# Kernel optimization log

Hardware: AMD Instinct MI355X
Metric: run time of the kernel (lower is better)

## Reference

```python
import math
import jax, jax.numpy as jnp
import numpy as np

B, L, D, H, DFF = 2, 2048, 1024, 16, 4096
HD = D // H
NUM_BUCKETS, MAX_DISTANCE = 32, 128


def setup_inputs() -> dict:
    key = jax.random.key(0)
    ks = jax.random.split(key, 10)
    s = 0.02
    return {
        "hidden_states": jax.random.normal(ks[0], (B, L, D), dtype=jnp.float32),
        "Wq": jax.random.normal(ks[1], (D, D), dtype=jnp.float32) * s,
        "Wk": jax.random.normal(ks[2], (D, D), dtype=jnp.float32) * s,
        "Wv": jax.random.normal(ks[3], (D, D), dtype=jnp.float32) * s,
        "Wo": jax.random.normal(ks[4], (D, D), dtype=jnp.float32) * s,
        "W1": jax.random.normal(ks[5], (D, DFF), dtype=jnp.float32) * s,
        "W2": jax.random.normal(ks[6], (DFF, D), dtype=jnp.float32) * s,
        "ln1_g": jnp.ones((D,), dtype=jnp.float32),
        "ln2_g": jnp.ones((D,), dtype=jnp.float32),
        "rel_table": jax.random.normal(ks[7], (NUM_BUCKETS, H), dtype=jnp.float32) * s,
    }


def rms_norm(x, g, eps=1e-6):
    # T5-style LayerNorm: scale only, no mean subtraction
    var = jnp.mean(jnp.square(x.astype(jnp.float32)), axis=-1, keepdims=True)
    return (x.astype(jnp.float32) * jax.lax.rsqrt(var + eps)).astype(x.dtype) * g


def relative_position_bias(seq_len, table):
    # bidirectional T5 bucket scheme, num_buckets=32, max_distance=128
    ctx = jnp.arange(seq_len)[:, None]
    mem = jnp.arange(seq_len)[None, :]
    rp = mem - ctx                                  # (L, L) int
    nb = NUM_BUCKETS // 2
    buckets = (rp > 0).astype(jnp.int32) * nb
    rpa = jnp.abs(rp)
    max_exact = nb // 2
    is_small = rpa < max_exact
    safe = jnp.maximum(rpa, 1).astype(jnp.float32)  # avoid log(0); masked by is_small
    large = max_exact + (
        jnp.log(safe / max_exact) / math.log(MAX_DISTANCE / max_exact) * (nb - max_exact)
    ).astype(jnp.int32)
    large = jnp.minimum(large, nb - 1)
    buckets = buckets + jnp.where(is_small, rpa, large)   # (L, L)
    vals = table[buckets]                                  # (L, L, H)
    return jnp.transpose(vals, (2, 0, 1))[None]            # (1, H, L, L)


def reference(hidden_states, Wq, Wk, Wv, Wo, W1, W2, ln1_g, ln2_g, rel_table):
    x = hidden_states
    b, l, d = x.shape

    # --- self-attention sublayer (pre-norm) ---
    h = rms_norm(x, ln1_g)
    q = (h @ Wq).reshape(b, l, H, HD)
    k = (h @ Wk).reshape(b, l, H, HD)
    v = (h @ Wv).reshape(b, l, H, HD)

    bias = relative_position_bias(l, rel_table)            # (1, H, L, L)
    # NOTE: source's manual attention path has NO 1/sqrt(head_dim) scaling
    scores = jnp.einsum("bqhd,bkhd->bhqk", q, k) + bias
    attn = jax.nn.softmax(scores.astype(jnp.float32), axis=-1).astype(scores.dtype)
    out = jnp.einsum("bhqk,bkhd->bqhd", attn, v).reshape(b, l, d)
    x = x + out @ Wo

    # --- feed-forward sublayer (pre-norm) ---
    h = rms_norm(x, ln2_g)
    x = x + jax.nn.relu(h @ W1) @ W2
    return x
```

## Files before the change

kernel.cpp:

```cpp
#include <hip/hip_runtime.h>
#include <hip/hip_bf16.h>
#include <math.h>

#define BDIM 1024
#define HEADS 16
#define HDIM 64
#define LSEQ 2048
#define NBATCH 2
#define DFFDIM 4096
#define QKVN 3072

typedef __bf16 bf16x8_t __attribute__((ext_vector_type(8)));
typedef float f32x4_t __attribute__((ext_vector_type(4)));

__device__ __forceinline__ ushort f2bf(float f) {
    union { __hip_bfloat16 b; ushort u; } cv;
    cv.b = __float2bfloat16(f);
    return cv.u;
}
__device__ __forceinline__ float bf2f(ushort u) {
    union { unsigned int i; float f; } cv;
    cv.i = ((unsigned int)u) << 16;
    return cv.f;
}

__global__ __launch_bounds__(256) void transpose_cvt(const float* __restrict__ W,
                                                     ushort* __restrict__ Wt,
                                                     int K, int N) {
    __shared__ ushort tile[32][33];
    int bi = blockIdx.y;
    int bj = blockIdx.x;
    int tx = threadIdx.x;
    int ty = threadIdx.y;
#pragma unroll
    for (int r = 0; r < 4; ++r) {
        int krow = bi * 32 + ty + r * 8;
        int ncol = bj * 32 + tx;
        tile[ty + r * 8][tx] = f2bf(W[(size_t)krow * N + ncol]);
    }
    __syncthreads();
#pragma unroll
    for (int r = 0; r < 4; ++r) {
        int nrow = bj * 32 + ty + r * 8;
        int kcol = bi * 32 + tx;
        Wt[(size_t)nrow * K + kcol] = tile[tx][ty + r * 8];
    }
}

__global__ __launch_bounds__(256) void vtrans(const ushort* __restrict__ qkv,
                                              ushort* __restrict__ vT) {
    __shared__ ushort t[64][72];
    const int ktile = blockIdx.x;
    const int bh = blockIdx.y;
    const int b = bh >> 4, h = bh & 15;
    const int tid = threadIdx.x;
    const int r = tid >> 2;
    const int c0 = (tid & 3) * 16;
    const ushort* src = qkv + (size_t)(b * LSEQ + ktile * 64 + r) * QKVN + 2048 + h * HDIM + c0;
    union { bf16x8_t v; ushort s[8]; } u0, u1;
    u0.v = *(const bf16x8_t*)src;
    u1.v = *(const bf16x8_t*)(src + 8);
#pragma unroll
    for (int j = 0; j < 8; ++j) { t[r][c0 + j] = u0.s[j]; t[r][c0 + 8 + j] = u1.s[j]; }
    __syncthreads();
    const int hd = tid >> 2;
    union { bf16x8_t v; ushort s[8]; } w0, w1;
#pragma unroll
    for (int j = 0; j < 8; ++j) { w0.s[j] = t[c0 + j][hd]; w1.s[j] = t[c0 + 8 + j][hd]; }
    ushort* dst = vT + (size_t)(bh * HDIM + hd) * LSEQ + ktile * 64 + c0;
    *(bf16x8_t*)dst = w0.v;
    *(bf16x8_t*)(dst + 8) = w1.v;
}

__global__ __launch_bounds__(256) void rmsnorm_k(const float* __restrict__ x,
                                                 const float* __restrict__ g,
                                                 ushort* __restrict__ out) {
    int row = blockIdx.x;
    int t = threadIdx.x;
    int w = t >> 6, l = t & 63;
    const float4 v = reinterpret_cast<const float4*>(x + (size_t)row * BDIM)[t];
    float ss = v.x * v.x + v.y * v.y + v.z * v.z + v.w * v.w;
#pragma unroll
    for (int m = 1; m <= 32; m <<= 1) ss += __shfl_xor(ss, m);
    __shared__ float wsum[4];
    if (l == 0) wsum[w] = ss;
    __syncthreads();
    float tot = wsum[0] + wsum[1] + wsum[2] + wsum[3];
    float r = rsqrtf(tot * (1.0f / BDIM) + 1e-6f);
    const float4 gv = reinterpret_cast<const float4*>(g)[t];
    ushort4 o;
    o.x = f2bf(v.x * r * gv.x);
    o.y = f2bf(v.y * r * gv.y);
    o.z = f2bf(v.z * r * gv.z);
    o.w = f2bf(v.w * r * gv.w);
    reinterpret_cast<ushort4*>(out + (size_t)row * BDIM)[t] = o;
}

__global__ void bias_table_k(const float* __restrict__ rel, float* __restrict__ btab) {
    int idx = blockIdx.x * 256 + threadIdx.x;
    if (idx >= HEADS * 4095) return;
    int h = idx / 4095;
    int d = idx % 4095;
    int rp = d - 2047;
    int bucket = rp > 0 ? 16 : 0;
    int rpa = rp < 0 ? -rp : rp;
    if (rpa < 8) {
        bucket += rpa;
    } else {
        int large = 8 + (int)(logf((float)rpa * 0.125f) * (1.0f / logf(16.0f)) * 8.0f);
        bucket += large < 15 ? large : 15;
    }
    btab[idx] = rel[bucket * HEADS + h];
}

__global__ __launch_bounds__(256) void reduce2_k(const ushort* __restrict__ parts,
                                                 const float* __restrict__ res,
                                                 float* __restrict__ out,
                                                 size_t mn) {
    size_t i = ((size_t)blockIdx.x * 256 + threadIdx.x) * 4;
    float4 r = *(const float4*)(res + i);
    ushort4 a = *(const ushort4*)(parts + i);
    ushort4 b = *(const ushort4*)(parts + mn + i);
    float4 o;
    o.x = r.x + bf2f(a.x) + bf2f(b.x);
    o.y = r.y + bf2f(a.y) + bf2f(b.y);
    o.z = r.z + bf2f(a.z) + bf2f(b.z);
    o.w = r.w + bf2f(a.w) + bf2f(b.w);
    *(float4*)(out + i) = o;
}

__global__ __launch_bounds__(256) void reduce2_rms(const ushort* __restrict__ parts,
                                                   const float* __restrict__ res,
                                                   const float* __restrict__ g,
                                                   float* __restrict__ out,
                                                   ushort* __restrict__ hout,
                                                   size_t mn) {
    int row = blockIdx.x;
    int t = threadIdx.x;
    int w = t >> 6, l = t & 63;
    size_t i = (size_t)row * BDIM + t * 4;
    float4 r = *(const float4*)(res + i);
    ushort4 a = *(const ushort4*)(parts + i);
    ushort4 b = *(const ushort4*)(parts + mn + i);
    float4 o;
    o.x = r.x + bf2f(a.x) + bf2f(b.x);
    o.y = r.y + bf2f(a.y) + bf2f(b.y);
    o.z = r.z + bf2f(a.z) + bf2f(b.z);
    o.w = r.w + bf2f(a.w) + bf2f(b.w);
    *(float4*)(out + i) = o;
    float ss = o.x * o.x + o.y * o.y + o.z * o.z + o.w * o.w;
#pragma unroll
    for (int m = 1; m <= 32; m <<= 1) ss += __shfl_xor(ss, m);
    __shared__ float wsum[4];
    if (l == 0) wsum[w] = ss;
    __syncthreads();
    float tot = wsum[0] + wsum[1] + wsum[2] + wsum[3];
    float rr = rsqrtf(tot * (1.0f / BDIM) + 1e-6f);
    const float4 gv = reinterpret_cast<const float4*>(g)[t];
    ushort4 h;
    h.x = f2bf(o.x * rr * gv.x);
    h.y = f2bf(o.y * rr * gv.y);
    h.z = f2bf(o.z * rr * gv.z);
    h.w = f2bf(o.w * rr * gv.w);
    reinterpret_cast<ushort4*>(hout + (size_t)row * BDIM)[t] = h;
}

template <int MODE, int TM, int TN>
__global__ __launch_bounds__(256) void gemm_bt(const ushort* __restrict__ A,
                                               const ushort* __restrict__ Bt,
                                               void* Cout, const float* res,
                                               int M, int N, int K, int nbx, int nkc) {
    __shared__ __align__(16) ushort As[TM * 64];
    __shared__ __align__(16) ushort Bs[TN * 64];
    constexpr int MF = TM / 32, NF = TN / 32;
    const int nwg = gridDim.x;
    const int bid = blockIdx.x;
    const int swz = (bid & 7) * (nwg >> 3) + (bid >> 3);
    const int nxy = nwg / nkc;
    const int chunk = swz / nxy;
    const int bxy = swz % nxy;
    const int bx = bxy % nbx, by = bxy / nbx;
    const int Kc = K / nkc;
    const int kbeg = chunk * Kc;
    const int tid = threadIdx.x;
    const int w = tid >> 6, l = tid & 63;
    const int wm = w >> 1, wn = w & 1;
    const int rowA0 = by * TM;
    const int colB0 = bx * TN;
    const int lr = l >> 3;
    const int scs = ((l & 7) ^ lr) * 8;
    const int c = l & 15, gq = l >> 4;
    const int rswz = (c & 7) * 8;
    f32x4_t acc[MF][NF] = {};

    auto stage = [&](int k0) {
#pragma unroll
        for (int i = 0; i < TM / 32; ++i) {
            int r = i * 32 + w * 8;
            __builtin_amdgcn_global_load_lds(
                (const __attribute__((address_space(1))) uint32_t*)(A + (size_t)(rowA0 + r + lr) * K + kbeg + k0 + scs),
                (__attribute__((address_space(3))) uint32_t*)(&As[r * 64]), 16, 0, 0);
        }
#pragma unroll
        for (int i = 0; i < TN / 32; ++i) {
            int r = i * 32 + w * 8;
            __builtin_amdgcn_global_load_lds(
                (const __attribute__((address_space(1))) uint32_t*)(Bt + (size_t)(colB0 + r + lr) * K + kbeg + k0 + scs),
                (__attribute__((address_space(3))) uint32_t*)(&Bs[r * 64]), 16, 0, 0);
        }
    };

    const int nk = Kc >> 6;
    for (int kt = 0; kt < nk; ++kt) {
        __syncthreads();
        stage(kt << 6);
        __syncthreads();
#pragma unroll
        for (int kk = 0; kk < 2; ++kk) {
            bf16x8_t av[MF], bv[NF];
#pragma unroll
            for (int mf = 0; mf < MF; ++mf)
                av[mf] = *(const bf16x8_t*)&As[(wm * (TM / 2) + mf * 16 + c) * 64 + ((kk * 32 + gq * 8) ^ rswz)];
#pragma unroll
            for (int nf = 0; nf < NF; ++nf)
                bv[nf] = *(const bf16x8_t*)&Bs[(wn * (TN / 2) + nf * 16 + c) * 64 + ((kk * 32 + gq * 8) ^ rswz)];
#pragma unroll
            for (int mf = 0; mf < MF; ++mf)
#pragma unroll
                for (int nf = 0; nf < NF; ++nf)
                    acc[mf][nf] = __builtin_amdgcn_mfma_f32_16x16x32_bf16(av[mf], bv[nf], acc[mf][nf], 0, 0, 0);
        }
    }
#pragma unroll
    for (int mf = 0; mf < MF; ++mf) {
#pragma unroll
        for (int nf = 0; nf < NF; ++nf) {
#pragma unroll
            for (int i = 0; i < 4; ++i) {
                int row = rowA0 + wm * (TM / 2) + mf * 16 + gq * 4 + i;
                int col = colB0 + wn * (TN / 2) + nf * 16 + c;
                size_t idx = (size_t)row * N + col;
                float vv = acc[mf][nf][i];
                if (MODE == 0) {
                    ((ushort*)Cout)[idx] = f2bf(vv);
                } else if (MODE == 1) {
                    ((float*)Cout)[idx] = res[idx] + vv;
                } else if (MODE == 2) {
                    ((ushort*)Cout)[idx] = f2bf(vv > 0.f ? vv : 0.f);
                } else {
                    ((ushort*)Cout)[(size_t)chunk * M * N + idx] = f2bf(vv);
                }
            }
        }
    }
}

__global__ __launch_bounds__(512) void attn_fwd(const ushort* __restrict__ qkv,
                                                const ushort* __restrict__ vT,
                                                const float* __restrict__ btab,
                                                ushort* __restrict__ ob) {
    const int tid = threadIdx.x, w = tid >> 6, l = tid & 63;
    const int bh = blockIdx.y, b = bh >> 4, h = bh & 15;
    const int qt = blockIdx.x;
    __shared__ __align__(16) ushort Ks[2][64 * 64];
    __shared__ __align__(16) ushort Vs[2][64 * 64];
    __shared__ __align__(16) ushort Pl[8][16 * 72];
    const int q0 = qt * 128 + w * 16;
    const int c = l & 15, g = l >> 4;
    const size_t rowbase = (size_t)b * LSEQ * QKVN;
    const ushort* qp = qkv + rowbase + h * HDIM;
    const ushort* kp = qkv + rowbase + BDIM + h * HDIM;
    const ushort* vtp = vT + (size_t)bh * HDIM * LSEQ;
    const int sr = tid >> 3;
    const int scs = ((l & 7) ^ (l >> 3)) * 8;
    const float* btq4 = btab + h * 4095 + 2047 - (q0 + c) + g * 4;

    bf16x8_t aq[2];
#pragma unroll
    for (int kk = 0; kk < 2; ++kk)
        aq[kk] = *(const bf16x8_t*)(qp + (size_t)(q0 + c) * QKVN + kk * 32 + g * 8);

    float lrow = 0.f;
    f32x4_t o[4] = {};
    f32x4_t s[4];

    auto stage = [&](int buf, int key0) {
        __builtin_amdgcn_global_load_lds(
            (const __attribute__((address_space(1))) uint32_t*)(kp + (size_t)(key0 + sr) * QKVN + scs),
            (__attribute__((address_space(3))) uint32_t*)(&Ks[buf][(w * 8) * 64]), 16, 0, 0);
        __builtin_amdgcn_global_load_lds(
            (const __attribute__((address_space(1))) uint32_t*)(vtp + (size_t)sr * LSEQ + key0 + scs),
            (__attribute__((address_space(3))) uint32_t*)(&Vs[buf][(w * 8) * 64]), 16, 0, 0);
    };
    auto loadBias = [&](int key0) {
#pragma unroll
        for (int nf = 0; nf < 4; ++nf)
#pragma unroll
            for (int i = 0; i < 4; ++i)
                s[nf][i] = btq4[key0 + nf * 16 + i];
    };

    stage(0, 0);
    loadBias(0);
    int cur = 0;

    ushort* Pw = Pl[w];
    const int rswz = (c & 7) << 3;
    for (int kt = 0; kt < 32; ++kt) {
        __syncthreads();
        if (kt < 31) stage(cur ^ 1, kt * 64 + 64);
#pragma unroll
        for (int kk = 0; kk < 2; ++kk)
#pragma unroll
            for (int nf = 0; nf < 4; ++nf) {
                bf16x8_t kf = *(const bf16x8_t*)&Ks[cur][(nf * 16 + c) * 64 + ((kk * 32 + g * 8) ^ rswz)];
                s[nf] = __builtin_amdgcn_mfma_f32_16x16x32_bf16(kf, aq[kk], s[nf], 0, 0, 0);
            }
        float rs = 0.f;
        union { ushort us[4]; uint2 u2; } pk[4];
#pragma unroll
        for (int nf = 0; nf < 4; ++nf)
#pragma unroll
            for (int i = 0; i < 4; ++i) {
                float pv = __expf(s[nf][i]);
                rs += pv;
                pk[nf].us[i] = f2bf(pv);
            }
        if (kt < 31) loadBias(kt * 64 + 64);
        lrow += rs;
#pragma unroll
        for (int nf = 0; nf < 4; ++nf)
            *(uint2*)&Pw[c * 72 + nf * 16 + g * 4] = pk[nf].u2;
        bf16x8_t pa[2];
#pragma unroll
        for (int kk = 0; kk < 2; ++kk)
            pa[kk] = *(const bf16x8_t*)&Pw[c * 72 + kk * 32 + g * 8];
#pragma unroll
        for (int kk = 0; kk < 2; ++kk)
#pragma unroll
            for (int hf = 0; hf < 4; ++hf) {
                bf16x8_t vf = *(const bf16x8_t*)&Vs[cur][(hf * 16 + c) * 64 + ((kk * 32 + g * 8) ^ rswz)];
                o[hf] = __builtin_amdgcn_mfma_f32_16x16x32_bf16(vf, pa[kk], o[hf], 0, 0, 0);
            }
        cur ^= 1;
    }
    lrow += __shfl_xor(lrow, 16);
    lrow += __shfl_xor(lrow, 32);
    const float inv = 1.f / lrow;
    ushort* orow = ob + (size_t)(b * LSEQ + q0 + c) * BDIM + h * HDIM + g * 4;
#pragma unroll
    for (int hf = 0; hf < 4; ++hf) {
        ushort4 ov;
        ov.x = f2bf(o[hf][0] * inv);
        ov.y = f2bf(o[hf][1] * inv);
        ov.z = f2bf(o[hf][2] * inv);
        ov.w = f2bf(o[hf][3] * inv);
        *(ushort4*)(orow + hf * 16) = ov;
    }
}

extern "C" void kernel_launch(void* const* d_in, const int* in_sizes, int n_in,
                              void* d_out, int out_size, void* d_ws, size_t ws_size,
                              hipStream_t stream) {
    const float* x   = (const float*)d_in[0];
    const float* Wq  = (const float*)d_in[1];
    const float* Wk  = (const float*)d_in[2];
    const float* Wv  = (const float*)d_in[3];
    const float* Wo  = (const float*)d_in[4];
    const float* W1  = (const float*)d_in[5];
    const float* W2  = (const float*)d_in[6];
    const float* g1  = (const float*)d_in[7];
    const float* g2  = (const float*)d_in[8];
    const float* rel = (const float*)d_in[9];
    float* out = (float*)d_out;

    char* ws = (char*)d_ws;
    const size_t MB = 1024 * 1024;
    ushort* wqkvT = (ushort*)(ws + 0 * MB);
    ushort* woT   = (ushort*)(ws + 6 * MB);
    ushort* w1T   = (ushort*)(ws + 8 * MB);
    ushort* w2T   = (ushort*)(ws + 16 * MB);
    float*  btab  = (float*)(ws + 24 * MB);
    ushort* hbuf  = (ushort*)(ws + 25 * MB);
    ushort* qkvb  = (ushort*)(ws + 33 * MB);
    ushort* woP   = (ushort*)(ws + 33 * MB);
    ushort* f1b   = (ushort*)(ws + 33 * MB);
    ushort* vTb   = (ushort*)(ws + 57 * MB);
    ushort* w2P   = (ushort*)(ws + 0 * MB);
    (void)in_sizes; (void)n_in; (void)out_size; (void)ws_size;

    const size_t MN = (size_t)4096 * 1024;
    dim3 tb(32, 8);
    transpose_cvt<<<dim3(32, 32),  tb, 0, stream>>>(Wq, wqkvT,                1024, 1024);
    transpose_cvt<<<dim3(32, 32),  tb, 0, stream>>>(Wk, wqkvT + 1024 * 1024,  1024, 1024);
    transpose_cvt<<<dim3(32, 32),  tb, 0, stream>>>(Wv, wqkvT + 2048 * 1024,  1024, 1024);
    transpose_cvt<<<dim3(32, 32),  tb, 0, stream>>>(Wo, woT, 1024, 1024);
    transpose_cvt<<<dim3(128, 32), tb, 0, stream>>>(W1, w1T, 1024, 4096);
    transpose_cvt<<<dim3(32, 128), tb, 0, stream>>>(W2, w2T, 4096, 1024);
    bias_table_k<<<256, 256, 0, stream>>>(rel, btab);

    rmsnorm_k<<<4096, 256, 0, stream>>>(x, g1, hbuf);
    gemm_bt<0, 128, 128><<<768, 256, 0, stream>>>(hbuf, wqkvT, qkvb, nullptr, 4096, QKVN, 1024, 24, 1);
    vtrans<<<dim3(32, 32), 256, 0, stream>>>(qkvb, vTb);
    attn_fwd<<<dim3(16, 32), 512, 0, stream>>>(qkvb, vTb, btab, hbuf);
    gemm_bt<3, 128, 128><<<512, 256, 0, stream>>>(hbuf, woT, woP, nullptr, 4096, 1024, 1024, 8, 2);
    reduce2_rms<<<4096, 256, 0, stream>>>(woP, x, g2, out, hbuf, MN);
    gemm_bt<2, 128, 128><<<1024, 256, 0, stream>>>(hbuf, w1T, f1b, nullptr, 4096, DFFDIM, 1024, 32, 1);
    gemm_bt<3, 128, 128><<<512, 256, 0, stream>>>(f1b, w2T, w2P, nullptr, 4096, 1024, 4096, 8, 2);
    reduce2_k<<<4096, 256, 0, stream>>>(w2P, out, out, MN);
}
```

Before: 244.3 us.

## Split attention over two key halves with a combine kernel; batch square weight transposes

Attention now runs as a split-K (flash-decoding style) kernel: each block handles half of the keys and writes unnormalised partial outputs in bf16 plus row sums, and a new combine kernel adds the two halves and normalises. This doubles the attention grid from 512 to 1024 blocks to fill more compute units. The cost is an extra kernel launch, extra global traffic for the partial outputs, and an extra bf16 rounding step. Separately, the four 1024x1024 weight transpose launches are merged into one 3D-grid launch to cut launch overhead.

New measurement: 248.6 us. Within noise of the previous version (+1.8%).

```diff
diff --git a/kernel.cpp b/kernel.cpp
--- a/kernel.cpp
+++ b/kernel.cpp
@@ -45,6 +45,29 @@
         int kcol = bi * 32 + tx;
         Wt[(size_t)nrow * K + kcol] = tile[tx][ty + r * 8];
     }
+}
+
+__global__ __launch_bounds__(256) void transpose_cvt4(const float* __restrict__ W0,
+                                                      const float* __restrict__ W1,
+                                                      const float* __restrict__ W2,
+                                                      const float* __restrict__ W3,
+                                                      ushort* __restrict__ T0,
+                                                      ushort* __restrict__ T1,
+                                                      ushort* __restrict__ T2,
+                                                      ushort* __restrict__ T3) {
+    __shared__ ushort tile[32][33];
+    const int z = blockIdx.z;
+    const float* W = z == 0 ? W0 : z == 1 ? W1 : z == 2 ? W2 : W3;
+    ushort* T = z == 0 ? T0 : z == 1 ? T1 : z == 2 ? T2 : T3;
+    int bi = blockIdx.y, bj = blockIdx.x;
+    int tx = threadIdx.x, ty = threadIdx.y;
+#pragma unroll
+    for (int r = 0; r < 4; ++r)
+        tile[ty + r * 8][tx] = f2bf(W[(size_t)(bi * 32 + ty + r * 8) * 1024 + bj * 32 + tx]);
+    __syncthreads();
+#pragma unroll
+    for (int r = 0; r < 4; ++r)
+        T[(size_t)(bj * 32 + ty + r * 8) * 1024 + bi * 32 + tx] = tile[tx][ty + r * 8];
 }
 
 __global__ __launch_bounds__(256) void vtrans(const ushort* __restrict__ qkv,
@@ -255,13 +278,16 @@
     }
 }
 
-__global__ __launch_bounds__(512) void attn_fwd(const ushort* __restrict__ qkv,
-                                                const ushort* __restrict__ vT,
-                                                const float* __restrict__ btab,
-                                                ushort* __restrict__ ob) {
+__global__ __launch_bounds__(512) void attn_fwd_split(const ushort* __restrict__ qkv,
+                                                      const ushort* __restrict__ vT,
+                                                      const float* __restrict__ btab,
+                                                      ushort* __restrict__ opart,
+                                                      float* __restrict__ lpart) {
     const int tid = threadIdx.x, w = tid >> 6, l = tid & 63;
     const int bh = blockIdx.y, b = bh >> 4, h = bh & 15;
     const int qt = blockIdx.x;
+    const int half = blockIdx.z;
+    const int keybase = half * 1024;
     __shared__ __align__(16) ushort Ks[2][64 * 64];
     __shared__ __align__(16) ushort Vs[2][64 * 64];
     __shared__ __align__(16) ushort Pl[8][16 * 72];
@@ -300,15 +326,16 @@
                 s[nf][i] = btq4[key0 + nf * 16 + i];
     };
 
-    stage(0, 0);
-    loadBias(0);
+    stage(0, keybase);
+    loadBias(keybase);
     int cur = 0;
 
     ushort* Pw = Pl[w];
     const int rswz = (c & 7) << 3;
-    for (int kt = 0; kt < 32; ++kt) {
+    for (int kt = 0; kt < 16; ++kt) {
+        const int key0 = keybase + kt * 64;
         __syncthreads();
-        if (kt < 31) stage(cur ^ 1, kt * 64 + 64);
+        if (kt < 15) stage(cur ^ 1, key0 + 64);
 #pragma unroll
         for (int kk = 0; kk < 2; ++kk)
 #pragma unroll
@@ -326,7 +353,7 @@
                 rs += pv;
                 pk[nf].us[i] = f2bf(pv);
             }
-        if (kt < 31) loadBias(kt * 64 + 64);
+        if (kt < 15) loadBias(key0 + 64);
         lrow += rs;
 #pragma unroll
         for (int nf = 0; nf < 4; ++nf)
@@ -346,17 +373,38 @@
     }
     lrow += __shfl_xor(lrow, 16);
     lrow += __shfl_xor(lrow, 32);
-    const float inv = 1.f / lrow;
-    ushort* orow = ob + (size_t)(b * LSEQ + q0 + c) * BDIM + h * HDIM + g * 4;
+    ushort* orow = opart + (size_t)half * 4194304 + (size_t)(b * LSEQ + q0 + c) * BDIM + h * HDIM + g * 4;
 #pragma unroll
     for (int hf = 0; hf < 4; ++hf) {
         ushort4 ov;
-        ov.x = f2bf(o[hf][0] * inv);
-        ov.y = f2bf(o[hf][1] * inv);
-        ov.z = f2bf(o[hf][2] * inv);
-        ov.w = f2bf(o[hf][3] * inv);
+        ov.x = f2bf(o[hf][0]);
+        ov.y = f2bf(o[hf][1]);
+        ov.z = f2bf(o[hf][2]);
+        ov.w = f2bf(o[hf][3]);
         *(ushort4*)(orow + hf * 16) = ov;
     }
+    if (l < 16) lpart[half * 65536 + bh * 2048 + q0 + c] = lrow;
+}
+
+__global__ __launch_bounds__(256) void attn_combine(const ushort* __restrict__ opart,
+                                                    const float* __restrict__ lpart,
+                                                    ushort* __restrict__ ob) {
+    const int row = blockIdx.x;
+    const int t = threadIdx.x;
+    const int b = row >> 11, q = row & 2047;
+    const int h = t >> 4;
+    const float denom = lpart[(b * 16 + h) * 2048 + q] +
+                        lpart[65536 + (b * 16 + h) * 2048 + q];
+    const float inv = 1.f / denom;
+    size_t i = (size_t)row * BDIM + t * 4;
+    ushort4 a = *(const ushort4*)(opart + i);
+    ushort4 c = *(const ushort4*)(opart + 4194304 + i);
+    ushort4 o;
+    o.x = f2bf((bf2f(a.x) + bf2f(c.x)) * inv);
+    o.y = f2bf((bf2f(a.y) + bf2f(c.y)) * inv);
+    o.z = f2bf((bf2f(a.z) + bf2f(c.z)) * inv);
+    o.w = f2bf((bf2f(a.w) + bf2f(c.w)) * inv);
+    *(ushort4*)(ob + i) = o;
 }
 
 extern "C" void kernel_launch(void* const* d_in, const int* in_sizes, int n_in,
@@ -386,15 +434,15 @@
     ushort* woP   = (ushort*)(ws + 33 * MB);
     ushort* f1b   = (ushort*)(ws + 33 * MB);
     ushort* vTb   = (ushort*)(ws + 57 * MB);
+    ushort* oPrt  = (ushort*)(ws + 65 * MB);
+    float*  lPrt  = (float*)(ws + 81 * MB);
     ushort* w2P   = (ushort*)(ws + 0 * MB);
     (void)in_sizes; (void)n_in; (void)out_size; (void)ws_size;
 
     const size_t MN = (size_t)4096 * 1024;
     dim3 tb(32, 8);
-    transpose_cvt<<<dim3(32, 32),  tb, 0, stream>>>(Wq, wqkvT,                1024, 1024);
-    transpose_cvt<<<dim3(32, 32),  tb, 0, stream>>>(Wk, wqkvT + 1024 * 1024,  1024, 1024);
-    transpose_cvt<<<dim3(32, 32),  tb, 0, stream>>>(Wv, wqkvT + 2048 * 1024,  1024, 1024);
-    transpose_cvt<<<dim3(32, 32),  tb, 0, stream>>>(Wo, woT, 1024, 1024);
+    transpose_cvt4<<<dim3(32, 32, 4), tb, 0, stream>>>(Wq, Wk, Wv, Wo,
+        wqkvT, wqkvT + 1024 * 1024, wqkvT + 2048 * 1024, woT);
     transpose_cvt<<<dim3(128, 32), tb, 0, stream>>>(W1, w1T, 1024, 4096);
     transpose_cvt<<<dim3(32, 128), tb, 0, stream>>>(W2, w2T, 4096, 1024);
     bias_table_k<<<256, 256, 0, stream>>>(rel, btab);
@@ -402,7 +450,8 @@
     rmsnorm_k<<<4096, 256, 0, stream>>>(x, g1, hbuf);
     gemm_bt<0, 128, 128><<<768, 256, 0, stream>>>(hbuf, wqkvT, qkvb, nullptr, 4096, QKVN, 1024, 24, 1);
     vtrans<<<dim3(32, 32), 256, 0, stream>>>(qkvb, vTb);
-    attn_fwd<<<dim3(16, 32), 512, 0, stream>>>(qkvb, vTb, btab, hbuf);
+    attn_fwd_split<<<dim3(16, 32, 2), 512, 0, stream>>>(qkvb, vTb, btab, oPrt, lPrt);
+    attn_combine<<<4096, 256, 0, stream>>>(oPrt, lPrt, hbuf);
     gemm_bt<3, 128, 128><<<512, 256, 0, stream>>>(hbuf, woT, woP, nullptr, 4096, 1024, 1024, 8, 2);
     reduce2_rms<<<4096, 256, 0, stream>>>(woP, x, g2, out, hbuf, MN);
     gemm_bt<2, 128, 128><<<1024, 256, 0, stream>>>(hbuf, w1T, f1b, nullptr, 4096, DFFDIM, 1024, 32, 1);
```

## Add 256x256-tile 8-wave GEMM for FFN up-projection and batch weight transposes

Applied to the files above, without the earlier changes.

Adds a new GEMM kernel with 256x256 output tiles, 512 threads, double-buffered direct global-to-LDS loads, swizzled LDS reads and interleaved prefetch barriers. It is used for the W1 up-projection with ReLU in place of the 128x128 kernel, to raise operand reuse per tile. The four square weight transpose-convert launches are also merged into one launch with a z-dimension, cutting launch overhead. The large tile uses 128KB of LDS and runs one block per CU, and the 256-block grid gives roughly one wave of work on the device, so any load imbalance is exposed.

New measurement: 229.1 us. 1.07x faster.

```diff
diff --git a/kernel.cpp b/kernel.cpp
--- a/kernel.cpp
+++ b/kernel.cpp
@@ -45,6 +45,29 @@
         int kcol = bi * 32 + tx;
         Wt[(size_t)nrow * K + kcol] = tile[tx][ty + r * 8];
     }
+}
+
+__global__ __launch_bounds__(256) void transpose_cvt4(const float* __restrict__ W0,
+                                                      const float* __restrict__ W1,
+                                                      const float* __restrict__ W2,
+                                                      const float* __restrict__ W3,
+                                                      ushort* __restrict__ T0,
+                                                      ushort* __restrict__ T1,
+                                                      ushort* __restrict__ T2,
+                                                      ushort* __restrict__ T3) {
+    __shared__ ushort tile[32][33];
+    const int z = blockIdx.z;
+    const float* W = z == 0 ? W0 : z == 1 ? W1 : z == 2 ? W2 : W3;
+    ushort* T = z == 0 ? T0 : z == 1 ? T1 : z == 2 ? T2 : T3;
+    int bi = blockIdx.y, bj = blockIdx.x;
+    int tx = threadIdx.x, ty = threadIdx.y;
+#pragma unroll
+    for (int r = 0; r < 4; ++r)
+        tile[ty + r * 8][tx] = f2bf(W[(size_t)(bi * 32 + ty + r * 8) * 1024 + bj * 32 + tx]);
+    __syncthreads();
+#pragma unroll
+    for (int r = 0; r < 4; ++r)
+        T[(size_t)(bj * 32 + ty + r * 8) * 1024 + bi * 32 + tx] = tile[tx][ty + r * 8];
 }
 
 __global__ __launch_bounds__(256) void vtrans(const ushort* __restrict__ qkv,
@@ -255,6 +278,102 @@
     }
 }
 
+template <int MODE>
+__global__ __launch_bounds__(512, 1) void gemm_bt8(const ushort* __restrict__ A,
+                                                   const ushort* __restrict__ Bt,
+                                                   void* Cout,
+                                                   int M, int N, int K, int nbx) {
+    __shared__ __align__(16) ushort As[2][256 * 64];
+    __shared__ __align__(16) ushort Bs[2][256 * 64];
+    const int nwg = gridDim.x;
+    const int bid = blockIdx.x;
+    const int swz = (bid & 7) * (nwg >> 3) + (bid >> 3);
+    const int bx = swz % nbx, by = swz / nbx;
+    const int tid = threadIdx.x;
+    const int w = tid >> 6, l = tid & 63;
+    const int wm = w >> 2, wn = w & 3;
+    const int rowA0 = by * 256, colB0 = bx * 256;
+    const int st_r = tid >> 3;
+    const int scs = ((l & 7) ^ (st_r & 7)) * 8;
+    const int c = l & 15, gq = l >> 4;
+    const int rswz = (c & 7) * 8;
+    f32x4_t acc[8][4] = {};
+
+    auto stageChunk = [&](int buf, int k0, int q) {
+        __builtin_amdgcn_global_load_lds(
+            (const __attribute__((address_space(1))) uint32_t*)(A + (size_t)(rowA0 + q * 64 + st_r) * K + k0 + scs),
+            (__attribute__((address_space(3))) uint32_t*)(&As[buf][(q * 64 + w * 8) * 64]), 16, 0, 0);
+        __builtin_amdgcn_global_load_lds(
+            (const __attribute__((address_space(1))) uint32_t*)(Bt + (size_t)(colB0 + q * 64 + st_r) * K + k0 + scs),
+            (__attribute__((address_space(3))) uint32_t*)(&Bs[buf][(q * 64 + w * 8) * 64]), 16, 0, 0);
+    };
+
+    const int nk = K >> 6;
+    stageChunk(0, 0, 0);
+    stageChunk(0, 0, 1);
+    stageChunk(0, 0, 2);
+    stageChunk(0, 0, 3);
+    asm volatile("s_waitcnt vmcnt(0)" ::: "memory");
+    __builtin_amdgcn_s_barrier();
+    __builtin_amdgcn_sched_barrier(0);
+
+    for (int k = 0; k < nk; ++k) {
+        const int cur = k & 1;
+        const ushort* Ab = &As[cur][0];
+        const ushort* Bb = &Bs[cur][0];
+#pragma unroll
+        for (int q = 0; q < 4; ++q) {
+            const int mh = q >> 1, nh = q & 1;
+            bf16x8_t av[4][2], bv[2][2];
+#pragma unroll
+            for (int mf = 0; mf < 4; ++mf)
+#pragma unroll
+                for (int kk = 0; kk < 2; ++kk)
+                    av[mf][kk] = *(const bf16x8_t*)&Ab[(wm * 128 + mh * 64 + mf * 16 + c) * 64 + ((kk * 32 + gq * 8) ^ rswz)];
+#pragma unroll
+            for (int nf = 0; nf < 2; ++nf)
+#pragma unroll
+                for (int kk = 0; kk < 2; ++kk)
+                    bv[nf][kk] = *(const bf16x8_t*)&Bb[(wn * 64 + nh * 32 + nf * 16 + c) * 64 + ((kk * 32 + gq * 8) ^ rswz)];
+            if (k + 1 < nk) stageChunk(cur ^ 1, (k + 1) << 6, q);
+            __builtin_amdgcn_s_barrier();
+            __builtin_amdgcn_sched_barrier(0);
+            __builtin_amdgcn_s_setprio(1);
+#pragma unroll
+            for (int kk = 0; kk < 2; ++kk)
+#pragma unroll
+                for (int mf = 0; mf < 4; ++mf)
+#pragma unroll
+                    for (int nf = 0; nf < 2; ++nf)
+                        acc[mh * 4 + mf][nh * 2 + nf] = __builtin_amdgcn_mfma_f32_16x16x32_bf16(
+                            av[mf][kk], bv[nf][kk], acc[mh * 4 + mf][nh * 2 + nf], 0, 0, 0);
+            __builtin_amdgcn_s_setprio(0);
+            if (q == 3 && k + 1 < nk)
+                asm volatile("s_waitcnt vmcnt(0)" ::: "memory");
+            __builtin_amdgcn_s_barrier();
+            __builtin_amdgcn_sched_barrier(0);
+        }
+    }
+#pragma unroll
+    for (int am = 0; am < 8; ++am) {
+#pragma unroll
+        for (int an = 0; an < 4; ++an) {
+#pragma unroll
+            for (int i = 0; i < 4; ++i) {
+                int row = rowA0 + wm * 128 + am * 16 + gq * 4 + i;
+                int col = colB0 + wn * 64 + an * 16 + c;
+                size_t idx = (size_t)row * N + col;
+                float vv = acc[am][an][i];
+                if (MODE == 0) {
+                    ((ushort*)Cout)[idx] = f2bf(vv);
+                } else {
+                    ((ushort*)Cout)[idx] = f2bf(vv > 0.f ? vv : 0.f);
+                }
+            }
+        }
+    }
+}
+
 __global__ __launch_bounds__(512) void attn_fwd(const ushort* __restrict__ qkv,
                                                 const ushort* __restrict__ vT,
                                                 const float* __restrict__ btab,
@@ -391,10 +510,8 @@
 
     const size_t MN = (size_t)4096 * 1024;
     dim3 tb(32, 8);
-    transpose_cvt<<<dim3(32, 32),  tb, 0, stream>>>(Wq, wqkvT,                1024, 1024);
-    transpose_cvt<<<dim3(32, 32),  tb, 0, stream>>>(Wk, wqkvT + 1024 * 1024,  1024, 1024);
-    transpose_cvt<<<dim3(32, 32),  tb, 0, stream>>>(Wv, wqkvT + 2048 * 1024,  1024, 1024);
-    transpose_cvt<<<dim3(32, 32),  tb, 0, stream>>>(Wo, woT, 1024, 1024);
+    transpose_cvt4<<<dim3(32, 32, 4), tb, 0, stream>>>(Wq, Wk, Wv, Wo,
+        wqkvT, wqkvT + 1024 * 1024, wqkvT + 2048 * 1024, woT);
     transpose_cvt<<<dim3(128, 32), tb, 0, stream>>>(W1, w1T, 1024, 4096);
     transpose_cvt<<<dim3(32, 128), tb, 0, stream>>>(W2, w2T, 4096, 1024);
     bias_table_k<<<256, 256, 0, stream>>>(rel, btab);
@@ -405,7 +522,7 @@
     attn_fwd<<<dim3(16, 32), 512, 0, stream>>>(qkvb, vTb, btab, hbuf);
     gemm_bt<3, 128, 128><<<512, 256, 0, stream>>>(hbuf, woT, woP, nullptr, 4096, 1024, 1024, 8, 2);
     reduce2_rms<<<4096, 256, 0, stream>>>(woP, x, g2, out, hbuf, MN);
-    gemm_bt<2, 128, 128><<<1024, 256, 0, stream>>>(hbuf, w1T, f1b, nullptr, 4096, DFFDIM, 1024, 32, 1);
+    gemm_bt8<2><<<256, 512, 0, stream>>>(hbuf, w1T, f1b, 4096, DFFDIM, 1024, 16);
     gemm_bt<3, 128, 128><<<512, 256, 0, stream>>>(f1b, w2T, w2P, nullptr, 4096, 1024, 4096, 8, 2);
     reduce2_k<<<4096, 256, 0, stream>>>(w2P, out, out, MN);
 }
```
